# Kernel optimization log

Hardware: AMD Instinct MI355X
Metric: run time of the kernel (lower is better)

Reference implementation:

```python
import jax, jax.numpy as jnp
import numpy as np

B, H, S, D = 2, 16, 2048, 128
NEG = -1.0e9  # matches masked_fill_(-1000000000.0)


def setup_inputs() -> dict:
    key = jax.random.key(0)
    kq, kk, kv = jax.random.split(key, 3)
    Q = jax.random.normal(kq, (B, H, S, D), dtype=jnp.float32)
    K = jax.random.normal(kk, (B, H, S, D), dtype=jnp.float32)
    V = jax.random.normal(kv, (B, H, S, D), dtype=jnp.float32)
    # causal mask: True means masked (filled with -1e9)
    causal = jnp.triu(jnp.ones((S, S), dtype=jnp.bool_), k=1)
    attn_mask = jnp.broadcast_to(causal, (B, H, S, S))
    return {"Q": Q, "K": K, "V": V, "attn_mask": attn_mask}


def reference(Q, K, V, attn_mask):
    d_k = K.shape[-1]
    scale = 1.0 / np.sqrt(d_k).astype(np.float32)
    # [B,H,S,S]
    scores = jnp.einsum('bhqd,bhkd->bhqk', Q, K) * scale
    scores = jnp.where(attn_mask, NEG, scores)
    attn = jax.nn.softmax(scores, axis=-1)
    # dropout p=0.0 -> identity
    context = jnp.einsum('bhqk,bhkd->bhqd', attn, V)
    return context
```

## Files before the change

### kernel.cpp

```cpp
#include <hip/hip_runtime.h>
#include <hip/hip_bf16.h>


#define S_LEN 2048
#define D_DIM 128
#define QTILE 64
#define KTILE 32
#define SCALE 0.08838834764831845f

typedef __attribute__((ext_vector_type(8))) short short8;
typedef __attribute__((ext_vector_type(4))) short short4v;
typedef __attribute__((ext_vector_type(4))) float float4v;

#define KROW 136
#define VROW 40
#define PROW 40
#define KS_OFF 0
#define VT_OFF 4352
#define PS_OFF 9472
#define LDS_SHORTS 12032

static __device__ __forceinline__ short f2bs(float f) {
    union { __hip_bfloat16 h; short s; } u;
    u.h = __float2bfloat16(f);
    return u.s;
}

__global__ __launch_bounds__(256, 4)
void sdpa_causal_kernel(const float* __restrict__ Qg,
                        const float* __restrict__ Kg,
                        const float* __restrict__ Vg,
                        float* __restrict__ Og) {
    __shared__ __align__(16) short lds[LDS_SHORTS];
    short* Ks = lds + KS_OFF;
    short* Vt = lds + VT_OFF;
    short* Ps = lds + PS_OFF;

    const int t    = threadIdx.x;
    const int w    = t >> 6;
    const int l    = t & 63;
    const int lc   = l & 15;
    const int quad = l >> 4;

    const int id = blockIdx.x;
    const int a  = id >> 3;
    const int bh = ((id & 7) << 2) + (a >> 4);
    const int pr = a & 15;

    const size_t base = (size_t)bh * S_LEN * D_DIM;

    const int kkey0 = t >> 5;
    const int kd0   = (t & 31) << 2;
    const int vkey  = t & 31;

    short8 ones;
    {
        const short v = (lc == 0) ? (short)0x3F80 : (short)0;
        for (int j = 0; j < 8; ++j) ones[j] = v;
    }

    for (int pass = 0; pass < 2; ++pass) {
        const int qt = pass ? pr : (31 - pr);
        const int qbase = qt * QTILE;
        const int q0    = qbase + w * 16;

        short8 qa[4];
        {
            const float* qp = Qg + base + (size_t)(q0 + lc) * D_DIM;
            for (int kc = 0; kc < 4; ++kc) {
                const float4* p = (const float4*)(qp + kc * 32 + quad * 8);
                float4 x0 = p[0];
                float4 x1 = p[1];
                short8 f;
                f[0] = f2bs(x0.x * SCALE); f[1] = f2bs(x0.y * SCALE);
                f[2] = f2bs(x0.z * SCALE); f[3] = f2bs(x0.w * SCALE);
                f[4] = f2bs(x1.x * SCALE); f[5] = f2bs(x1.y * SCALE);
                f[6] = f2bs(x1.z * SCALE); f[7] = f2bs(x1.w * SCALE);
                qa[kc] = f;
            }
        }

        float4v o[8];
        for (int n = 0; n < 8; ++n) o[n] = (float4v){0.f, 0.f, 0.f, 0.f};
        float4v ol = (float4v){0.f, 0.f, 0.f, 0.f};

        const int ntiles = 2 * qt + 2;

        float4 kreg[4], vreg[4];
        for (int g = 0; g < 4; ++g) {
            kreg[g] = *(const float4*)(Kg + base + (size_t)(kkey0 + 8 * g) * D_DIM + kd0);
            vreg[g] = *(const float4*)(Vg + base + (size_t)vkey * D_DIM + 4 * (kkey0 + 8 * g));
        }

        for (int kt = 0; kt < ntiles; ++kt) {
            const int kbase = kt * KTILE;

            __syncthreads();

            for (int g = 0; g < 4; ++g) {
                short4v ks = { f2bs(kreg[g].x), f2bs(kreg[g].y),
                               f2bs(kreg[g].z), f2bs(kreg[g].w) };
                *(short4v*)&Ks[(kkey0 + 8 * g) * KROW + kd0] = ks;
                const int vd = 4 * (kkey0 + 8 * g);
                Vt[(vd + 0) * VROW + vkey] = f2bs(vreg[g].x);
                Vt[(vd + 1) * VROW + vkey] = f2bs(vreg[g].y);
                Vt[(vd + 2) * VROW + vkey] = f2bs(vreg[g].z);
                Vt[(vd + 3) * VROW + vkey] = f2bs(vreg[g].w);
            }

            if (kt + 1 < ntiles) {
                const size_t koff = base + (size_t)(kt + 1) * KTILE * D_DIM;
                for (int g = 0; g < 4; ++g) {
                    kreg[g] = *(const float4*)(Kg + koff + (size_t)(kkey0 + 8 * g) * D_DIM + kd0);
                    vreg[g] = *(const float4*)(Vg + koff + (size_t)vkey * D_DIM + 4 * (kkey0 + 8 * g));
                }
            }

            __syncthreads();

            if (kbase > q0 + 15) continue;

            float4v sf[2];
            sf[0] = (float4v){0.f, 0.f, 0.f, 0.f};
            sf[1] = (float4v){0.f, 0.f, 0.f, 0.f};
            for (int n = 0; n < 2; ++n) {
                const int krow = (n * 16 + lc) * KROW;
                for (int kc = 0; kc < 4; ++kc) {
                    short8 kb = *(const short8*)&Ks[krow + kc * 32 + quad * 8];
                    sf[n] = __builtin_amdgcn_mfma_f32_16x16x32_bf16(qa[kc], kb, sf[n], 0, 0, 0);
                }
            }

            if (kbase + 31 > q0) {
                for (int n = 0; n < 2; ++n) {
                    const int key = kbase + n * 16 + lc;
                    for (int r = 0; r < 4; ++r)
                        if (key > q0 + quad * 4 + r) sf[n][r] = -INFINITY;
                }
            }

            for (int n = 0; n < 2; ++n)
                for (int r = 0; r < 4; ++r)
                    sf[n][r] = __expf(sf[n][r]);

            short* Pw = Ps + w * 16 * PROW;
            for (int n = 0; n < 2; ++n)
                for (int r = 0; r < 4; ++r)
                    Pw[(quad * 4 + r) * PROW + n * 16 + lc] = f2bs(sf[n][r]);
            __asm__ volatile("" ::: "memory");
            short8 pa = *(const short8*)&Pw[lc * PROW + quad * 8];

            for (int n = 0; n < 8; ++n) {
                short8 vb = *(const short8*)&Vt[(n * 16 + lc) * VROW + quad * 8];
                o[n] = __builtin_amdgcn_mfma_f32_16x16x32_bf16(pa, vb, o[n], 0, 0, 0);
            }
            ol = __builtin_amdgcn_mfma_f32_16x16x32_bf16(pa, ones, ol, 0, 0, 0);
        }

        float inv[4];
        for (int r = 0; r < 4; ++r)
            inv[r] = 1.0f / __shfl(ol[r], l & 48);
        const size_t ob = base + (size_t)q0 * D_DIM;
        for (int n = 0; n < 8; ++n)
            for (int r = 0; r < 4; ++r)
                Og[ob + (size_t)(quad * 4 + r) * D_DIM + n * 16 + lc] = o[n][r] * inv[r];
    }
}

extern "C" void kernel_launch(void* const* d_in, const int* in_sizes, int n_in,
                              void* d_out, int out_size, void* d_ws, size_t ws_size,
                              hipStream_t stream) {
    (void)in_sizes; (void)n_in; (void)d_ws; (void)ws_size; (void)out_size;
    const float* Qg = (const float*)d_in[0];
    const float* Kg = (const float*)d_in[1];
    const float* Vg = (const float*)d_in[2];
    float* Og = (float*)d_out;
    sdpa_causal_kernel<<<dim3(512), dim3(256), 0, stream>>>(Qg, Kg, Vg, Og);
}
```

Before: 762.7 us.

## Process both paired query tiles in one K/V sweep with 64-key tiles

Instead of two sequential passes that each stream K/V for one query tile, the block now holds Q fragments and accumulators for both paired tiles and streams K/V once, feeding the shorter tile only while it is still causal-active. The K tile grows to 64 keys with larger LDS buffers, and exp2f is used with log2e folded into the Q scale. The row-sum MFMA against a ones vector is replaced by per-lane accumulation plus a final shuffle reduction. This halves K/V global loads and conversions but doubles accumulator registers, and occupancy is lowered to 2 blocks per CU. There is also a block-index remap for the pair ordering.

```diff
diff --git a/kernel.cpp b/kernel.cpp
--- a/kernel.cpp
+++ b/kernel.cpp
@@ -4,21 +4,20 @@
 
 #define S_LEN 2048
 #define D_DIM 128
-#define QTILE 64
-#define KTILE 32
-#define SCALE 0.08838834764831845f
+#define KTILE 64
+#define QSCALE 0.12751743f
 
 typedef __attribute__((ext_vector_type(8))) short short8;
 typedef __attribute__((ext_vector_type(4))) short short4v;
 typedef __attribute__((ext_vector_type(4))) float float4v;
 
 #define KROW 136
-#define VROW 40
-#define PROW 40
+#define VROW 72
+#define PROW 72
 #define KS_OFF 0
-#define VT_OFF 4352
-#define PS_OFF 9472
-#define LDS_SHORTS 12032
+#define VT_OFF 8704
+#define PS_OFF 17920
+#define LDS_SHORTS 22528
 
 static __device__ __forceinline__ short f2bs(float f) {
     union { __hip_bfloat16 h; short s; } u;
@@ -26,7 +25,7 @@
     return u.s;
 }
 
-__global__ __launch_bounds__(256, 4)
+__global__ __launch_bounds__(256, 2)
 void sdpa_causal_kernel(const float* __restrict__ Qg,
                         const float* __restrict__ Kg,
                         const float* __restrict__ Vg,
@@ -42,129 +41,147 @@
     const int lc   = l & 15;
     const int quad = l >> 4;
 
-    const int id = blockIdx.x;
-    const int a  = id >> 3;
-    const int bh = ((id & 7) << 2) + (a >> 4);
-    const int pr = a & 15;
+    const int id  = blockIdx.x;
+    const int a   = id >> 3;
+    const int bh  = ((id & 7) << 2) + (a >> 4);
+    const int prr = a & 15;
+    const int pr  = (a & 32) ? (15 - prr) : prr;
+    const int qtA = 31 - pr;
+    const int qtB = pr;
 
     const size_t base = (size_t)bh * S_LEN * D_DIM;
 
-    const int kkey0 = t >> 5;
-    const int kd0   = (t & 31) << 2;
-    const int vkey  = t & 31;
+    const int q0A = qtA * 64 + w * 16;
+    const int q0B = qtB * 64 + w * 16;
 
-    short8 ones;
+    short8 qaA[4], qaB[4];
     {
-        const short v = (lc == 0) ? (short)0x3F80 : (short)0;
-        for (int j = 0; j < 8; ++j) ones[j] = v;
+        const float* qpA = Qg + base + (size_t)(q0A + lc) * D_DIM;
+        const float* qpB = Qg + base + (size_t)(q0B + lc) * D_DIM;
+        for (int kc = 0; kc < 4; ++kc) {
+            const float4* pA = (const float4*)(qpA + kc * 32 + quad * 8);
+            const float4* pB = (const float4*)(qpB + kc * 32 + quad * 8);
+            float4 a0 = pA[0], a1 = pA[1], b0 = pB[0], b1 = pB[1];
+            short8 fA, fB;
+            fA[0]=f2bs(a0.x*QSCALE); fA[1]=f2bs(a0.y*QSCALE);
+            fA[2]=f2bs(a0.z*QSCALE); fA[3]=f2bs(a0.w*QSCALE);
+            fA[4]=f2bs(a1.x*QSCALE); fA[5]=f2bs(a1.y*QSCALE);
+            fA[6]=f2bs(a1.z*QSCALE); fA[7]=f2bs(a1.w*QSCALE);
+            fB[0]=f2bs(b0.x*QSCALE); fB[1]=f2bs(b0.y*QSCALE);
+            fB[2]=f2bs(b0.z*QSCALE); fB[3]=f2bs(b0.w*QSCALE);
+            fB[4]=f2bs(b1.x*QSCALE); fB[5]=f2bs(b1.y*QSCALE);
+            fB[6]=f2bs(b1.z*QSCALE); fB[7]=f2bs(b1.w*QSCALE);
+            qaA[kc] = fA; qaB[kc] = fB;
+        }
     }
 
-    for (int pass = 0; pass < 2; ++pass) {
-        const int qt = pass ? pr : (31 - pr);
-        const int qbase = qt * QTILE;
-        const int q0    = qbase + w * 16;
+    float4v oA[8], oB[8];
+    for (int n = 0; n < 8; ++n) {
+        oA[n] = (float4v){0.f,0.f,0.f,0.f};
+        oB[n] = (float4v){0.f,0.f,0.f,0.f};
+    }
+    float lsA[4] = {0.f,0.f,0.f,0.f};
+    float lsB[4] = {0.f,0.f,0.f,0.f};
 
-        short8 qa[4];
-        {
-            const float* qp = Qg + base + (size_t)(q0 + lc) * D_DIM;
-            for (int kc = 0; kc < 4; ++kc) {
-                const float4* p = (const float4*)(qp + kc * 32 + quad * 8);
-                float4 x0 = p[0];
-                float4 x1 = p[1];
-                short8 f;
-                f[0] = f2bs(x0.x * SCALE); f[1] = f2bs(x0.y * SCALE);
-                f[2] = f2bs(x0.z * SCALE); f[3] = f2bs(x0.w * SCALE);
-                f[4] = f2bs(x1.x * SCALE); f[5] = f2bs(x1.y * SCALE);
-                f[6] = f2bs(x1.z * SCALE); f[7] = f2bs(x1.w * SCALE);
-                qa[kc] = f;
+    const int kk_t = t >> 5;
+    const int kd_t = (t & 31) << 2;
+    const int vk_t = t & 63;
+    const int vd_t = (t >> 6) << 3;
+
+    const int ntiles = qtA + 1;
+
+    float4 kreg[8], vreg[8];
+    for (int g = 0; g < 8; ++g) {
+        kreg[g] = *(const float4*)(Kg + base + (size_t)(kk_t + 8*g) * D_DIM + kd_t);
+        vreg[g] = *(const float4*)(Vg + base + (size_t)vk_t * D_DIM + 4*(vd_t + g));
+    }
+
+    auto computeTile = [&](const short8* qa, float4v* o, float* ls,
+                           int q0, int kb, bool straddle) {
+        float4v sf[4];
+        for (int n = 0; n < 4; ++n) {
+            const short* kr = &Ks[(n * 16 + lc) * KROW];
+            float4v s = (float4v){0.f,0.f,0.f,0.f};
+            for (int kc = 0; kc < 4; ++kc)
+                s = __builtin_amdgcn_mfma_f32_16x16x32_bf16(
+                        qa[kc], *(const short8*)&kr[kc * 32 + quad * 8], s, 0, 0, 0);
+            sf[n] = s;
+        }
+        if (straddle) {
+            for (int n = 0; n < 4; ++n) {
+                const int key = kb + n * 16 + lc;
+                for (int r = 0; r < 4; ++r)
+                    if (key > q0 + quad * 4 + r) sf[n][r] = -INFINITY;
+            }
+        }
+        for (int n = 0; n < 4; ++n)
+            for (int r = 0; r < 4; ++r) {
+                const float p = exp2f(sf[n][r]);
+                sf[n][r] = p;
+                ls[r] += p;
+            }
+        short* Pw = Ps + w * 16 * PROW;
+        for (int n = 0; n < 4; ++n)
+            for (int r = 0; r < 4; ++r)
+                Pw[(quad * 4 + r) * PROW + n * 16 + lc] = f2bs(sf[n][r]);
+        __asm__ volatile("" ::: "memory");
+        short8 pa0 = *(const short8*)&Pw[lc * PROW + quad * 8];
+        short8 pa1 = *(const short8*)&Pw[lc * PROW + 32 + quad * 8];
+        for (int nd = 0; nd < 8; ++nd) {
+            const short* vr = &Vt[(nd * 16 + lc) * VROW];
+            o[nd] = __builtin_amdgcn_mfma_f32_16x16x32_bf16(
+                        pa0, *(const short8*)&vr[quad * 8], o[nd], 0, 0, 0);
+            o[nd] = __builtin_amdgcn_mfma_f32_16x16x32_bf16(
+                        pa1, *(const short8*)&vr[32 + quad * 8], o[nd], 0, 0, 0);
+        }
+    };
+
+    for (int kt = 0; kt < ntiles; ++kt) {
+        const int kb = kt * KTILE;
+
+        __syncthreads();
+
+        for (int g = 0; g < 8; ++g) {
+            short4v ks = { f2bs(kreg[g].x), f2bs(kreg[g].y),
+                           f2bs(kreg[g].z), f2bs(kreg[g].w) };
+            *(short4v*)&Ks[(kk_t + 8*g) * KROW + kd_t] = ks;
+            const int vd = 4 * (vd_t + g);
+            Vt[(vd + 0) * VROW + vk_t] = f2bs(vreg[g].x);
+            Vt[(vd + 1) * VROW + vk_t] = f2bs(vreg[g].y);
+            Vt[(vd + 2) * VROW + vk_t] = f2bs(vreg[g].z);
+            Vt[(vd + 3) * VROW + vk_t] = f2bs(vreg[g].w);
+        }
+
+        if (kt + 1 < ntiles) {
+            const size_t koff = base + (size_t)(kt + 1) * KTILE * D_DIM;
+            for (int g = 0; g < 8; ++g) {
+                kreg[g] = *(const float4*)(Kg + koff + (size_t)(kk_t + 8*g) * D_DIM + kd_t);
+                vreg[g] = *(const float4*)(Vg + koff + (size_t)vk_t * D_DIM + 4*(vd_t + g));
             }
         }
 
-        float4v o[8];
-        for (int n = 0; n < 8; ++n) o[n] = (float4v){0.f, 0.f, 0.f, 0.f};
-        float4v ol = (float4v){0.f, 0.f, 0.f, 0.f};
+        __syncthreads();
 
-        const int ntiles = 2 * qt + 2;
+        computeTile(qaA, oA, lsA, q0A, kb, kt == qtA);
+        if (kt <= qtB)
+            computeTile(qaB, oB, lsB, q0B, kb, kt == qtB);
+    }
 
-        float4 kreg[4], vreg[4];
-        for (int g = 0; g < 4; ++g) {
-            kreg[g] = *(const float4*)(Kg + base + (size_t)(kkey0 + 8 * g) * D_DIM + kd0);
-            vreg[g] = *(const float4*)(Vg + base + (size_t)vkey * D_DIM + 4 * (kkey0 + 8 * g));
+    auto storeO = [&](const float4v* o, const float* ls, int q0) {
+        float inv[4];
+        for (int r = 0; r < 4; ++r) {
+            float s = ls[r];
+            for (int mask = 1; mask < 16; mask <<= 1)
+                s += __shfl_xor(s, mask);
+            inv[r] = 1.0f / s;
         }
-
-        for (int kt = 0; kt < ntiles; ++kt) {
-            const int kbase = kt * KTILE;
-
-            __syncthreads();
-
-            for (int g = 0; g < 4; ++g) {
-                short4v ks = { f2bs(kreg[g].x), f2bs(kreg[g].y),
-                               f2bs(kreg[g].z), f2bs(kreg[g].w) };
-                *(short4v*)&Ks[(kkey0 + 8 * g) * KROW + kd0] = ks;
-                const int vd = 4 * (kkey0 + 8 * g);
-                Vt[(vd + 0) * VROW + vkey] = f2bs(vreg[g].x);
-                Vt[(vd + 1) * VROW + vkey] = f2bs(vreg[g].y);
-                Vt[(vd + 2) * VROW + vkey] = f2bs(vreg[g].z);
-                Vt[(vd + 3) * VROW + vkey] = f2bs(vreg[g].w);
-            }
-
-            if (kt + 1 < ntiles) {
-                const size_t koff = base + (size_t)(kt + 1) * KTILE * D_DIM;
-                for (int g = 0; g < 4; ++g) {
-                    kreg[g] = *(const float4*)(Kg + koff + (size_t)(kkey0 + 8 * g) * D_DIM + kd0);
-                    vreg[g] = *(const float4*)(Vg + koff + (size_t)vkey * D_DIM + 4 * (kkey0 + 8 * g));
-                }
-            }
-
-            __syncthreads();
-
-            if (kbase > q0 + 15) continue;
-
-            float4v sf[2];
-            sf[0] = (float4v){0.f, 0.f, 0.f, 0.f};
-            sf[1] = (float4v){0.f, 0.f, 0.f, 0.f};
-            for (int n = 0; n < 2; ++n) {
-                const int krow = (n * 16 + lc) * KROW;
-                for (int kc = 0; kc < 4; ++kc) {
-                    short8 kb = *(const short8*)&Ks[krow + kc * 32 + quad * 8];
-                    sf[n] = __builtin_amdgcn_mfma_f32_16x16x32_bf16(qa[kc], kb, sf[n], 0, 0, 0);
-                }
-            }
-
-            if (kbase + 31 > q0) {
-                for (int n = 0; n < 2; ++n) {
-                    const int key = kbase + n * 16 + lc;
-                    for (int r = 0; r < 4; ++r)
-                        if (key > q0 + quad * 4 + r) sf[n][r] = -INFINITY;
-                }
-            }
-
-            for (int n = 0; n < 2; ++n)
-                for (int r = 0; r < 4; ++r)
-                    sf[n][r] = __expf(sf[n][r]);
-
-            short* Pw = Ps + w * 16 * PROW;
-            for (int n = 0; n < 2; ++n)
-                for (int r = 0; r < 4; ++r)
-                    Pw[(quad * 4 + r) * PROW + n * 16 + lc] = f2bs(sf[n][r]);
-            __asm__ volatile("" ::: "memory");
-            short8 pa = *(const short8*)&Pw[lc * PROW + quad * 8];
-
-            for (int n = 0; n < 8; ++n) {
-                short8 vb = *(const short8*)&Vt[(n * 16 + lc) * VROW + quad * 8];
-                o[n] = __builtin_amdgcn_mfma_f32_16x16x32_bf16(pa, vb, o[n], 0, 0, 0);
-            }
-            ol = __builtin_amdgcn_mfma_f32_16x16x32_bf16(pa, ones, ol, 0, 0, 0);
-        }
-
-        float inv[4];
-        for (int r = 0; r < 4; ++r)
-            inv[r] = 1.0f / __shfl(ol[r], l & 48);
         const size_t ob = base + (size_t)q0 * D_DIM;
-        for (int n = 0; n < 8; ++n)
+        for (int nd = 0; nd < 8; ++nd)
             for (int r = 0; r < 4; ++r)
-                Og[ob + (size_t)(quad * 4 + r) * D_DIM + n * 16 + lc] = o[n][r] * inv[r];
-    }
+                Og[ob + (size_t)(quad * 4 + r) * D_DIM + nd * 16 + lc] = o[nd][r] * inv[r];
+    };
+    storeO(oA, lsA, q0A);
+    storeO(oB, lsB, q0B);
 }
 
 extern "C" void kernel_launch(void* const* d_in, const int* in_sizes, int n_in,
```

After: 719.3 us. 5.7% less time.
